# Optimization experiments

Hardware: AMD Instinct MI355X
Metric: run time of the kernel (lower is better)

The kernel has to match this reference:

```python
import jax, jax.numpy as jnp
import numpy as np

HEADS = 4
DIM_HEAD = 32
DIM = HEADS * DIM_HEAD  # 128
B, H, W, C = 32, 64, 64, 128
LN_EPS = 1e-5


def setup_inputs() -> dict:
    key = jax.random.key(0)
    k0, k1, k2, k3, k4 = jax.random.split(key, 5)
    x = jax.random.normal(k0, (B, H, W, C), dtype=jnp.float32)
    # 1x1 convs are pointwise dense layers over channels
    w_qkv = jax.random.normal(k1, (C, DIM * 3), dtype=jnp.float32) * (1.0 / np.sqrt(C))
    w_out = jax.random.normal(k2, (DIM, C), dtype=jnp.float32) * (1.0 / np.sqrt(DIM))
    b_out = jax.random.normal(k3, (C,), dtype=jnp.float32) * 0.01
    ln_scale = jnp.ones((C,), dtype=jnp.float32)
    return {"x": x, "w_qkv": w_qkv, "w_out": w_out, "b_out": b_out, "ln_scale": ln_scale}


def reference(x, w_qkv, w_out, b_out, ln_scale):
    b, h, w, c = x.shape
    n = h * w
    # qkv projection (1x1 conv, no bias)
    qkv = jnp.einsum('bhwc,cf->bhwf', x, w_qkv)  # [B,H,W,3*DIM]
    q, k, v = jnp.split(qkv, 3, axis=-1)
    # rearrange 'b x y (h d) -> b (x y) h d'
    q = q.reshape(b, n, HEADS, DIM_HEAD)
    k = k.reshape(b, n, HEADS, DIM_HEAD)
    v = v.reshape(b, n, HEADS, DIM_HEAD)
    q = jax.nn.softmax(q, axis=-1) * (1.0 / np.sqrt(DIM_HEAD))
    k = jax.nn.softmax(k, axis=1)  # softmax over spatial positions
    v = v * (1.0 / n)
    # per-head context: [B, heads, d, e]
    context = jnp.einsum('bnhd,bnhe->bhde', k, v)
    # out: 'b h d e, b n h d -> b h e n', then rearrange 'b h e (x y) -> b x y (h e)'
    out = jnp.einsum('bhde,bnhd->bnhe', context, q)  # [B, n, heads, e]
    out = out.reshape(b, h, w, DIM)  # channel order = (h e), matching rearrange
    # output 1x1 conv (with bias)
    out = jnp.einsum('bhwd,dc->bhwc', out, w_out) + b_out
    # LayerNorm over channels, eps=1e-5, no bias
    mu = jnp.mean(out, axis=-1, keepdims=True)
    var = jnp.mean(jnp.square(out - mu), axis=-1, keepdims=True)
    out = (out - mu) * jax.lax.rsqrt(var + LN_EPS) * ln_scale
    return out
```

## Files before the change

kernel.cpp:

```cpp
#include <hip/hip_runtime.h>
#include <hip/hip_bf16.h>

typedef __attribute__((ext_vector_type(4))) float f32x4;
typedef __attribute__((ext_vector_type(8))) short bf16x8;

#define OFF_QS    0ull
#define OFF_EK    33554432ull
#define OFF_VV    67108864ull
#define OFF_PCTX  100663296ull
#define OFF_PSE   109051904ull
#define OFF_CTXG  109314048ull
#define OFF_WQT   109576192ull
#define OFF_WOT   109674496ull

static __device__ __forceinline__ unsigned short f2bf(float f) {
  unsigned int u = __builtin_bit_cast(unsigned int, f);
  return (unsigned short)((u + 0x7fffu + ((u >> 16) & 1u)) >> 16);
}

static __device__ __forceinline__ void unpack8(uint4 u, float* p) {
  p[0] = __builtin_bit_cast(float, u.x << 16);
  p[1] = __builtin_bit_cast(float, u.x & 0xffff0000u);
  p[2] = __builtin_bit_cast(float, u.y << 16);
  p[3] = __builtin_bit_cast(float, u.y & 0xffff0000u);
  p[4] = __builtin_bit_cast(float, u.z << 16);
  p[5] = __builtin_bit_cast(float, u.z & 0xffff0000u);
  p[6] = __builtin_bit_cast(float, u.w << 16);
  p[7] = __builtin_bit_cast(float, u.w & 0xffff0000u);
}

__global__ __launch_bounds__(256) void k_prep(const float* __restrict__ wqkv,
                                              const float* __restrict__ wout,
                                              unsigned short* __restrict__ wqT,
                                              unsigned short* __restrict__ woT) {
  int idx = blockIdx.x * 256 + threadIdx.x;
  if (idx < 49152) {
    int f = idx >> 7, k = idx & 127;
    wqT[idx] = f2bf(wqkv[k * 384 + f]);
  } else {
    int j = idx - 49152;
    int c = j >> 7, k = j & 127;
    woT[j] = f2bf(wout[k * 128 + c]);
  }
}

__global__ __launch_bounds__(512, 2) void k_qkv(const float* __restrict__ x,
                                                const unsigned short* __restrict__ wqT,
                                                unsigned short* __restrict__ qs,
                                                unsigned short* __restrict__ ek,
                                                unsigned short* __restrict__ vv) {
  extern __shared__ char lds[];
  char* lds_w = lds;
  char* lds_a = lds + 98304;

  const int tid = threadIdx.x;
  const long rowbase = (long)blockIdx.x * 128;

  {
    const int4* src = (const int4*)wqT;
    int4* dst = (int4*)lds_w;
#pragma unroll
    for (int i = 0; i < 12; i++) {
      int u = tid + i * 512;
      dst[u ^ ((u >> 4) & 7)] = src[u];
    }
  }
  {
    const f32x4* src = (const f32x4*)(x + rowbase * 128);
#pragma unroll
    for (int i = 0; i < 8; i++) {
      int u = tid + i * 512;
      f32x4 val = src[u];
      ushort4 bq;
      bq.x = f2bf(val.x); bq.y = f2bf(val.y); bq.z = f2bf(val.z); bq.w = f2bf(val.w);
      int ba = (u * 8) ^ (((u >> 5) & 7) << 4);
      *(ushort4*)(lds_a + ba) = bq;
    }
  }
  __syncthreads();

  const int lane = tid & 63;
  const int g = lane >> 4, c = lane & 15;
  const int wave = tid >> 6;
  const int wm = wave >> 2, wf = wave & 3;

  f32x4 acc[4][6];
#pragma unroll
  for (int mt = 0; mt < 4; mt++)
#pragma unroll
    for (int ft = 0; ft < 6; ft++)
      acc[mt][ft] = (f32x4){0.f, 0.f, 0.f, 0.f};

#pragma unroll
  for (int kk = 0; kk < 4; kk++) {
    const int koff = (kk * 32 + g * 8) * 2;
    bf16x8 af[4], bfrag[6];
#pragma unroll
    for (int mt = 0; mt < 4; mt++) {
      int row = wm * 64 + mt * 16 + c;
      af[mt] = *(const bf16x8*)(lds_a + ((row * 256 + koff) ^ ((row & 7) << 4)));
    }
#pragma unroll
    for (int ft = 0; ft < 6; ft++) {
      int frow = wf * 96 + ft * 16 + c;
      bfrag[ft] = *(const bf16x8*)(lds_w + ((frow * 256 + koff) ^ ((frow & 7) << 4)));
    }
#pragma unroll
    for (int mt = 0; mt < 4; mt++)
#pragma unroll
      for (int ft = 0; ft < 6; ft++)
        acc[mt][ft] = __builtin_amdgcn_mfma_f32_16x16x32_bf16(af[mt], bfrag[ft], acc[mt][ft], 0, 0, 0);
  }

  const float RS32 = 0.17677669529663687f;
#pragma unroll
  for (int ch = 0; ch < 3; ch++) {
    int gc = wf * 96 + ch * 32;
    int sec = gc >> 7;
    int sc = gc & 127;
    unsigned short* dstp = (sec == 0) ? qs : (sec == 1 ? ek : vv);
#pragma unroll
    for (int mt = 0; mt < 4; mt++) {
      f32x4 a0 = acc[mt][2 * ch];
      f32x4 a1 = acc[mt][2 * ch + 1];
      long row0 = rowbase + wm * 64 + mt * 16 + g * 4;
      if (sec == 0) {
#pragma unroll
        for (int r = 0; r < 4; r++) {
          float e0 = __expf(a0[r]), e1 = __expf(a1[r]);
          float s = e0 + e1;
          s += __shfl_xor(s, 1); s += __shfl_xor(s, 2);
          s += __shfl_xor(s, 4); s += __shfl_xor(s, 8);
          float inv = RS32 / s;
          long base = (row0 + r) * 128 + sc + c;
          dstp[base]      = f2bf(e0 * inv);
          dstp[base + 16] = f2bf(e1 * inv);
        }
      } else if (sec == 1) {
#pragma unroll
        for (int r = 0; r < 4; r++) {
          long base = (row0 + r) * 128 + sc + c;
          dstp[base]      = f2bf(__expf(a0[r]));
          dstp[base + 16] = f2bf(__expf(a1[r]));
        }
      } else {
#pragma unroll
        for (int r = 0; r < 4; r++) {
          long base = (row0 + r) * 128 + sc + c;
          dstp[base]      = f2bf(a0[r]);
          dstp[base + 16] = f2bf(a1[r]);
        }
      }
    }
  }
}

__global__ __launch_bounds__(256) void k_ctx(const unsigned short* __restrict__ ek,
                                             const unsigned short* __restrict__ vv,
                                             float* __restrict__ pctx,
                                             float* __restrict__ pse) {
  extern __shared__ char lds[];
  float* ekc = (float*)lds;
  float* vcc = (float*)(lds + 32768);

  const int tid = threadIdx.x;
  const int chunk = blockIdx.x, b = blockIdx.y;
  const long row0 = (long)b * 4096 + chunk * 256;
  const int wave = tid >> 6, lane = tid & 63;
  const int d0 = (lane >> 3) * 4, e0 = (lane & 7) * 4;
  const int nn = tid >> 2, part = tid & 3;

  f32x4 acc0 = {0.f,0.f,0.f,0.f}, acc1 = {0.f,0.f,0.f,0.f};
  f32x4 acc2 = {0.f,0.f,0.f,0.f}, acc3 = {0.f,0.f,0.f,0.f};
  f32x4 se   = {0.f,0.f,0.f,0.f};

  for (int s = 0; s < 4; s++) {
    long r = row0 + s * 64 + nn;
#pragma unroll
    for (int h = 0; h < 4; h++) {
      uint4 ue = *(const uint4*)(ek + r * 128 + h * 32 + part * 8);
      uint4 uv = *(const uint4*)(vv + r * 128 + h * 32 + part * 8);
      unpack8(ue, &ekc[(h * 64 + nn) * 32 + part * 8]);
      unpack8(uv, &vcc[(h * 64 + nn) * 32 + part * 8]);
    }
    __syncthreads();
    const float* eb = &ekc[(wave * 64) * 32];
    const float* vb = &vcc[(wave * 64) * 32];
#pragma unroll 4
    for (int n = 0; n < 64; n++) {
      f32x4 ev  = *(const f32x4*)(eb + n * 32 + d0);
      f32x4 v4  = *(const f32x4*)(vb + n * 32 + e0);
      acc0 += ev.x * v4;
      acc1 += ev.y * v4;
      acc2 += ev.z * v4;
      acc3 += ev.w * v4;
      se += ev;
    }
    __syncthreads();
  }
  const long pb = ((long)chunk * 128 + b * 4 + wave) * 1024;
  *(f32x4*)&pctx[pb + (d0 + 0) * 32 + e0] = acc0;
  *(f32x4*)&pctx[pb + (d0 + 1) * 32 + e0] = acc1;
  *(f32x4*)&pctx[pb + (d0 + 2) * 32 + e0] = acc2;
  *(f32x4*)&pctx[pb + (d0 + 3) * 32 + e0] = acc3;
  if ((lane & 7) == 0)
    *(f32x4*)&pse[((long)chunk * 128 + b * 4 + wave) * 32 + d0] = se;
}

__global__ __launch_bounds__(256) void k_ctxred(const float* __restrict__ pctx,
                                                const float* __restrict__ pse,
                                                unsigned short* __restrict__ ctxg) {
  int idx = blockIdx.x * 256 + threadIdx.x;
  int de = idx & 1023, d = de >> 5, bh = idx >> 10;
  float s = 0.f, sume = 0.f;
#pragma unroll
  for (int ch = 0; ch < 16; ch++) {
    s    += pctx[(ch * 128 + bh) * 1024 + de];
    sume += pse[(ch * 128 + bh) * 32 + d];
  }
  ctxg[idx] = f2bf(s / (sume * 4096.0f));
}

__global__ __launch_bounds__(512, 2) void k_out(const unsigned short* __restrict__ qs,
                                                const unsigned short* __restrict__ ctxg,
                                                const unsigned short* __restrict__ woT,
                                                const float* __restrict__ bout,
                                                const float* __restrict__ lnsc,
                                                float* __restrict__ out) {
  extern __shared__ char lds[];
  char* lds_wo = lds;
  char* lds_at = lds + 32768;
  unsigned short* lds_cx = (unsigned short*)(lds + 65536);
  float* lds_bias  = (float*)(lds + 73728);
  float* lds_scale = (float*)(lds + 74240);

  const int tid = threadIdx.x;
  const long rowbase = (long)blockIdx.x * 128;
  const int b = blockIdx.x >> 5;

  {
    const int4* src = (const int4*)woT;
    int4* dst = (int4*)lds_wo;
#pragma unroll
    for (int i = 0; i < 4; i++) {
      int u = tid + i * 512;
      dst[u ^ ((u >> 4) & 7)] = src[u];
    }
  }
  {
    const unsigned int* src = (const unsigned int*)(ctxg + (long)b * 4096);
#pragma unroll
    for (int i = 0; i < 4; i++) {
      int u = tid + i * 512;
      unsigned int w = src[u];
      int j = u * 2;
      int e = j & 31, d = (j >> 5) & 31, h = j >> 10;
      lds_cx[(h * 32 + e) * 32 + d]     = (unsigned short)(w & 0xffffu);
      lds_cx[(h * 32 + e + 1) * 32 + d] = (unsigned short)(w >> 16);
    }
  }
  if (tid < 128) { lds_bias[tid] = bout[tid]; lds_scale[tid] = lnsc[tid]; }
  __syncthreads();

  const int lane = tid & 63, g = lane >> 4, c = lane & 15;
  const int wave = tid >> 6;

  f32x4 acc1[4][2];
#pragma unroll
  for (int h = 0; h < 4; h++) { acc1[h][0] = (f32x4){0.f,0.f,0.f,0.f}; acc1[h][1] = (f32x4){0.f,0.f,0.f,0.f}; }
  const unsigned short* qrow = qs + (rowbase + wave * 16 + c) * 128;
#pragma unroll
  for (int h = 0; h < 4; h++) {
    bf16x8 a = *(const bf16x8*)(qrow + h * 32 + g * 8);
#pragma unroll
    for (int et = 0; et < 2; et++) {
      bf16x8 bq = *(const bf16x8*)(lds_cx + (h * 32 + et * 16 + c) * 32 + g * 8);
      acc1[h][et] = __builtin_amdgcn_mfma_f32_16x16x32_bf16(a, bq, acc1[h][et], 0, 0, 0);
    }
  }
  {
    int rowl = wave * 16 + g * 4;
#pragma unroll
    for (int h = 0; h < 4; h++)
#pragma unroll
      for (int et = 0; et < 2; et++) {
        int col = (2 * h + et) * 16 + c;
#pragma unroll
        for (int r = 0; r < 4; r++) {
          int row = rowl + r;
          int ba = (row * 256 + col * 2) ^ ((row & 7) << 4);
          *(unsigned short*)(lds_at + ba) = f2bf(acc1[h][et][r]);
        }
      }
  }
  __syncthreads();

  f32x4 acc2[8];
#pragma unroll
  for (int ct = 0; ct < 8; ct++) acc2[ct] = (f32x4){0.f,0.f,0.f,0.f};
#pragma unroll
  for (int kk = 0; kk < 4; kk++) {
    int koff = (kk * 32 + g * 8) * 2;
    int arow = wave * 16 + c;
    bf16x8 a = *(const bf16x8*)(lds_at + ((arow * 256 + koff) ^ ((arow & 7) << 4)));
#pragma unroll
    for (int ct = 0; ct < 8; ct++) {
      int wrow = ct * 16 + c;
      bf16x8 bw = *(const bf16x8*)(lds_wo + ((wrow * 256 + koff) ^ ((wrow & 7) << 4)));
      acc2[ct] = __builtin_amdgcn_mfma_f32_16x16x32_bf16(a, bw, acc2[ct], 0, 0, 0);
    }
  }

  float biasv[8], scalev[8];
#pragma unroll
  for (int ct = 0; ct < 8; ct++) { biasv[ct] = lds_bias[ct * 16 + c]; scalev[ct] = lds_scale[ct * 16 + c]; }
#pragma unroll
  for (int ct = 0; ct < 8; ct++)
#pragma unroll
    for (int r = 0; r < 4; r++)
      acc2[ct][r] += biasv[ct];

#pragma unroll
  for (int r = 0; r < 4; r++) {
    float s = 0.f, ss = 0.f;
#pragma unroll
    for (int ct = 0; ct < 8; ct++) { float v = acc2[ct][r]; s += v; ss += v * v; }
    s  += __shfl_xor(s, 1);  s  += __shfl_xor(s, 2);  s  += __shfl_xor(s, 4);  s  += __shfl_xor(s, 8);
    ss += __shfl_xor(ss, 1); ss += __shfl_xor(ss, 2); ss += __shfl_xor(ss, 4); ss += __shfl_xor(ss, 8);
    float mu = s * 0.0078125f;
    float var = ss * 0.0078125f - mu * mu;
    float rstd = rsqrtf(var + 1e-5f);
    long row = rowbase + wave * 16 + g * 4 + r;
#pragma unroll
    for (int ct = 0; ct < 8; ct++)
      out[row * 128 + ct * 16 + c] = (acc2[ct][r] - mu) * rstd * scalev[ct];
  }
}

extern "C" void kernel_launch(void* const* d_in, const int* in_sizes, int n_in,
                              void* d_out, int out_size, void* d_ws, size_t ws_size,
                              hipStream_t stream) {
  (void)in_sizes; (void)n_in; (void)out_size; (void)ws_size;
  const float* x     = (const float*)d_in[0];
  const float* wqkv  = (const float*)d_in[1];
  const float* wout  = (const float*)d_in[2];
  const float* bo    = (const float*)d_in[3];
  const float* lnsc  = (const float*)d_in[4];
  float* out = (float*)d_out;

  char* ws = (char*)d_ws;
  unsigned short* qs   = (unsigned short*)(ws + OFF_QS);
  unsigned short* ek   = (unsigned short*)(ws + OFF_EK);
  unsigned short* vv   = (unsigned short*)(ws + OFF_VV);
  float*          pctx = (float*)(ws + OFF_PCTX);
  float*          pse  = (float*)(ws + OFF_PSE);
  unsigned short* ctxg = (unsigned short*)(ws + OFF_CTXG);
  unsigned short* wqT  = (unsigned short*)(ws + OFF_WQT);
  unsigned short* woT  = (unsigned short*)(ws + OFF_WOT);

  k_prep<<<dim3(256), dim3(256), 0, stream>>>(wqkv, wout, wqT, woT);
  k_qkv<<<dim3(1024), dim3(512), 131072, stream>>>(x, wqT, qs, ek, vv);
  k_ctx<<<dim3(16, 32), dim3(256), 65536, stream>>>(ek, vv, pctx, pse);
  k_ctxred<<<dim3(512), dim3(256), 0, stream>>>(pctx, pse, ctxg);
  k_out<<<dim3(1024), dim3(512), 74752, stream>>>(qs, ctxg, woT, bo, lnsc, out);
}
```

Measured before the change: 226.1 us.

## Fuse K/V context accumulation into QKV projection kernel via LDS and MFMA

The QKV projection kernel now also computes per-head exp(K)^T V partial context with MFMA, reading from an LDS transpose, plus the exp(K) column sums. This removes the global writes and re-reads of the ek and vv intermediates (64 MB of bf16) and drops the separate k_ctx kernel. Each block now handles 512 rows over four 128-row tiles and prefetches the next x tile into registers. The grid shrinks from 1024 to 256 blocks and each tile gains extra barriers, which may reduce occupancy and latency hiding.

```diff
diff --git a/kernel.cpp b/kernel.cpp
--- a/kernel.cpp
+++ b/kernel.cpp
@@ -5,28 +5,15 @@
 typedef __attribute__((ext_vector_type(8))) short bf16x8;
 
 #define OFF_QS    0ull
-#define OFF_EK    33554432ull
-#define OFF_VV    67108864ull
-#define OFF_PCTX  100663296ull
-#define OFF_PSE   109051904ull
-#define OFF_CTXG  109314048ull
-#define OFF_WQT   109576192ull
-#define OFF_WOT   109674496ull
+#define OFF_PCTX  33554432ull
+#define OFF_PSE   41943040ull
+#define OFF_CTXG  42205184ull
+#define OFF_WQT   42467328ull
+#define OFF_WOT   42565632ull
 
 static __device__ __forceinline__ unsigned short f2bf(float f) {
   unsigned int u = __builtin_bit_cast(unsigned int, f);
   return (unsigned short)((u + 0x7fffu + ((u >> 16) & 1u)) >> 16);
-}
-
-static __device__ __forceinline__ void unpack8(uint4 u, float* p) {
-  p[0] = __builtin_bit_cast(float, u.x << 16);
-  p[1] = __builtin_bit_cast(float, u.x & 0xffff0000u);
-  p[2] = __builtin_bit_cast(float, u.y << 16);
-  p[3] = __builtin_bit_cast(float, u.y & 0xffff0000u);
-  p[4] = __builtin_bit_cast(float, u.z << 16);
-  p[5] = __builtin_bit_cast(float, u.z & 0xffff0000u);
-  p[6] = __builtin_bit_cast(float, u.w << 16);
-  p[7] = __builtin_bit_cast(float, u.w & 0xffff0000u);
 }
 
 __global__ __launch_bounds__(256) void k_prep(const float* __restrict__ wqkv,
@@ -44,17 +31,20 @@
   }
 }
 
-__global__ __launch_bounds__(512, 2) void k_qkv(const float* __restrict__ x,
-                                                const unsigned short* __restrict__ wqT,
-                                                unsigned short* __restrict__ qs,
-                                                unsigned short* __restrict__ ek,
-                                                unsigned short* __restrict__ vv) {
+__global__ __launch_bounds__(512, 2) void k_qkv_fused(const float* __restrict__ x,
+                                                      const unsigned short* __restrict__ wqT,
+                                                      unsigned short* __restrict__ qs,
+                                                      float* __restrict__ pctx,
+                                                      float* __restrict__ pse) {
   extern __shared__ char lds[];
   char* lds_w = lds;
   char* lds_a = lds + 98304;
 
   const int tid = threadIdx.x;
-  const long rowbase = (long)blockIdx.x * 128;
+  const int beta = blockIdx.x;
+  const int lane = tid & 63, g = lane >> 4, c = lane & 15;
+  const int wave = tid >> 6, wm = wave >> 2, wf = wave & 3;
+  const int h_task = wave & 3, ns_task = wave >> 2;
 
   {
     const int4* src = (const int4*)wqT;
@@ -65,158 +55,184 @@
       dst[u ^ ((u >> 4) & 7)] = src[u];
     }
   }
-  {
-    const f32x4* src = (const f32x4*)(x + rowbase * 128);
-#pragma unroll
-    for (int i = 0; i < 8; i++) {
-      int u = tid + i * 512;
-      f32x4 val = src[u];
-      ushort4 bq;
-      bq.x = f2bf(val.x); bq.y = f2bf(val.y); bq.z = f2bf(val.z); bq.w = f2bf(val.w);
-      int ba = (u * 8) ^ (((u >> 5) & 7) << 4);
-      *(ushort4*)(lds_a + ba) = bq;
-    }
-  }
-  __syncthreads();
-
-  const int lane = tid & 63;
-  const int g = lane >> 4, c = lane & 15;
-  const int wave = tid >> 6;
-  const int wm = wave >> 2, wf = wave & 3;
-
-  f32x4 acc[4][6];
-#pragma unroll
-  for (int mt = 0; mt < 4; mt++)
-#pragma unroll
-    for (int ft = 0; ft < 6; ft++)
-      acc[mt][ft] = (f32x4){0.f, 0.f, 0.f, 0.f};
-
-#pragma unroll
-  for (int kk = 0; kk < 4; kk++) {
-    const int koff = (kk * 32 + g * 8) * 2;
-    bf16x8 af[4], bfrag[6];
-#pragma unroll
-    for (int mt = 0; mt < 4; mt++) {
-      int row = wm * 64 + mt * 16 + c;
-      af[mt] = *(const bf16x8*)(lds_a + ((row * 256 + koff) ^ ((row & 7) << 4)));
-    }
-#pragma unroll
-    for (int ft = 0; ft < 6; ft++) {
-      int frow = wf * 96 + ft * 16 + c;
-      bfrag[ft] = *(const bf16x8*)(lds_w + ((frow * 256 + koff) ^ ((frow & 7) << 4)));
-    }
+
+  f32x4 pre[8];
+  {
+    const f32x4* src = (const f32x4*)(x + (long)beta * 512 * 128);
+#pragma unroll
+    for (int i = 0; i < 8; i++) pre[i] = src[i * 512 + tid];
+  }
+
+  f32x4 cacc[2][2];
+#pragma unroll
+  for (int dt = 0; dt < 2; dt++)
+#pragma unroll
+    for (int et = 0; et < 2; et++) cacc[dt][et] = (f32x4){0.f, 0.f, 0.f, 0.f};
+  float seacc[3][2];
+#pragma unroll
+  for (int i = 0; i < 3; i++) { seacc[i][0] = 0.f; seacc[i][1] = 0.f; }
+
+  for (int t = 0; t < 4; t++) {
+    const long rowbase = ((long)beta * 4 + t) * 128;
+    __syncthreads();
+
+    {
+#pragma unroll
+      for (int i = 0; i < 8; i++) {
+        int u = i * 512 + tid;
+        f32x4 val = pre[i];
+        ushort4 bq;
+        bq.x = f2bf(val.x); bq.y = f2bf(val.y); bq.z = f2bf(val.z); bq.w = f2bf(val.w);
+        int ba = (u * 8) ^ (((u >> 5) & 7) << 4);
+        *(ushort4*)(lds_a + ba) = bq;
+      }
+    }
+    if (t < 3) {
+      const f32x4* src = (const f32x4*)(x + (rowbase + 128) * 128);
+#pragma unroll
+      for (int i = 0; i < 8; i++) pre[i] = src[i * 512 + tid];
+    }
+    __syncthreads();
+
+    f32x4 acc[4][6];
 #pragma unroll
     for (int mt = 0; mt < 4; mt++)
 #pragma unroll
-      for (int ft = 0; ft < 6; ft++)
-        acc[mt][ft] = __builtin_amdgcn_mfma_f32_16x16x32_bf16(af[mt], bfrag[ft], acc[mt][ft], 0, 0, 0);
-  }
-
-  const float RS32 = 0.17677669529663687f;
+      for (int ft = 0; ft < 6; ft++) acc[mt][ft] = (f32x4){0.f, 0.f, 0.f, 0.f};
+
+#pragma unroll
+    for (int kk = 0; kk < 4; kk++) {
+      const int koff = (kk * 32 + g * 8) * 2;
+      bf16x8 af[4], bfrag[6];
+#pragma unroll
+      for (int mt = 0; mt < 4; mt++) {
+        int row = wm * 64 + mt * 16 + c;
+        af[mt] = *(const bf16x8*)(lds_a + ((row * 256 + koff) ^ ((row & 7) << 4)));
+      }
+#pragma unroll
+      for (int ft = 0; ft < 6; ft++) {
+        int frow = wf * 96 + ft * 16 + c;
+        bfrag[ft] = *(const bf16x8*)(lds_w + ((frow * 256 + koff) ^ ((frow & 7) << 4)));
+      }
+#pragma unroll
+      for (int mt = 0; mt < 4; mt++)
+#pragma unroll
+        for (int ft = 0; ft < 6; ft++)
+          acc[mt][ft] = __builtin_amdgcn_mfma_f32_16x16x32_bf16(af[mt], bfrag[ft], acc[mt][ft], 0, 0, 0);
+    }
+    __syncthreads();
+
+    const float RS32 = 0.17677669529663687f;
+#pragma unroll
+    for (int half = 0; half < 2; half++) {
+#pragma unroll
+      for (int ch = 0; ch < 3; ch++) {
+        int gc = wf * 96 + ch * 32;
+        int sec = gc >> 7;
+        int sc = gc & 127;
+        int h = (gc & 127) >> 5;
+        if (sec == 0) {
+          if (half == 0) {
+#pragma unroll
+            for (int mt = 0; mt < 4; mt++) {
+              f32x4 a0 = acc[mt][2 * ch], a1 = acc[mt][2 * ch + 1];
+              long row0 = rowbase + wm * 64 + mt * 16 + g * 4;
+#pragma unroll
+              for (int r = 0; r < 4; r++) {
+                float e0 = __expf(a0[r]), e1 = __expf(a1[r]);
+                float s = e0 + e1;
+                s += __shfl_xor(s, 1); s += __shfl_xor(s, 2);
+                s += __shfl_xor(s, 4); s += __shfl_xor(s, 8);
+                float inv = RS32 / s;
+                long base = (row0 + r) * 128 + sc + c;
+                qs[base]      = f2bf(e0 * inv);
+                qs[base + 16] = f2bf(e1 * inv);
+              }
+            }
+          }
+        } else if (wm == half) {
+          char* tbase = lds_a + (sec == 1 ? 0 : 16384) + h * 4096;
+#pragma unroll
+          for (int mt = 0; mt < 4; mt++) {
+            f32x4 a0 = acc[mt][2 * ch], a1 = acc[mt][2 * ch + 1];
+#pragma unroll
+            for (int r = 0; r < 4; r++) {
+              int nl = mt * 16 + g * 4 + r;
+              float v0 = a0[r], v1 = a1[r];
+              if (sec == 1) {
+                v0 = __expf(v0); v1 = __expf(v1);
+                seacc[ch][0] += v0; seacc[ch][1] += v1;
+              }
+              *(unsigned short*)(tbase + ((c * 128 + nl * 2) ^ ((c & 7) << 4))) = f2bf(v0);
+              *(unsigned short*)(tbase + (((c + 16) * 128 + nl * 2) ^ ((c & 7) << 4))) = f2bf(v1);
+            }
+          }
+        }
+      }
+      __syncthreads();
+
+      {
+        const int noff = (ns_task * 32 + g * 8) * 2;
+        bf16x8 afr[2], bfr[2];
+#pragma unroll
+        for (int dt = 0; dt < 2; dt++) {
+          int row = dt * 16 + c;
+          afr[dt] = *(const bf16x8*)(lds_a + h_task * 4096 + ((row * 128 + noff) ^ ((c & 7) << 4)));
+        }
+#pragma unroll
+        for (int et = 0; et < 2; et++) {
+          int row = et * 16 + c;
+          bfr[et] = *(const bf16x8*)(lds_a + 16384 + h_task * 4096 + ((row * 128 + noff) ^ ((c & 7) << 4)));
+        }
+#pragma unroll
+        for (int dt = 0; dt < 2; dt++)
+#pragma unroll
+          for (int et = 0; et < 2; et++)
+            cacc[dt][et] = __builtin_amdgcn_mfma_f32_16x16x32_bf16(afr[dt], bfr[et], cacc[dt][et], 0, 0, 0);
+      }
+      __syncthreads();
+    }
+  }
+
+  {
+    const long pcbase = ((long)beta * 8 + h_task * 2 + ns_task) * 1024;
+#pragma unroll
+    for (int dt = 0; dt < 2; dt++)
+#pragma unroll
+      for (int et = 0; et < 2; et++)
+#pragma unroll
+        for (int r = 0; r < 4; r++)
+          pctx[pcbase + (dt * 16 + g * 4 + r) * 32 + et * 16 + c] = cacc[dt][et][r];
+  }
 #pragma unroll
   for (int ch = 0; ch < 3; ch++) {
     int gc = wf * 96 + ch * 32;
-    int sec = gc >> 7;
-    int sc = gc & 127;
-    unsigned short* dstp = (sec == 0) ? qs : (sec == 1 ? ek : vv);
-#pragma unroll
-    for (int mt = 0; mt < 4; mt++) {
-      f32x4 a0 = acc[mt][2 * ch];
-      f32x4 a1 = acc[mt][2 * ch + 1];
-      long row0 = rowbase + wm * 64 + mt * 16 + g * 4;
-      if (sec == 0) {
-#pragma unroll
-        for (int r = 0; r < 4; r++) {
-          float e0 = __expf(a0[r]), e1 = __expf(a1[r]);
-          float s = e0 + e1;
-          s += __shfl_xor(s, 1); s += __shfl_xor(s, 2);
-          s += __shfl_xor(s, 4); s += __shfl_xor(s, 8);
-          float inv = RS32 / s;
-          long base = (row0 + r) * 128 + sc + c;
-          dstp[base]      = f2bf(e0 * inv);
-          dstp[base + 16] = f2bf(e1 * inv);
-        }
-      } else if (sec == 1) {
-#pragma unroll
-        for (int r = 0; r < 4; r++) {
-          long base = (row0 + r) * 128 + sc + c;
-          dstp[base]      = f2bf(__expf(a0[r]));
-          dstp[base + 16] = f2bf(__expf(a1[r]));
-        }
-      } else {
-#pragma unroll
-        for (int r = 0; r < 4; r++) {
-          long base = (row0 + r) * 128 + sc + c;
-          dstp[base]      = f2bf(a0[r]);
-          dstp[base + 16] = f2bf(a1[r]);
-        }
-      }
-    }
-  }
-}
-
-__global__ __launch_bounds__(256) void k_ctx(const unsigned short* __restrict__ ek,
-                                             const unsigned short* __restrict__ vv,
-                                             float* __restrict__ pctx,
-                                             float* __restrict__ pse) {
-  extern __shared__ char lds[];
-  float* ekc = (float*)lds;
-  float* vcc = (float*)(lds + 32768);
-
-  const int tid = threadIdx.x;
-  const int chunk = blockIdx.x, b = blockIdx.y;
-  const long row0 = (long)b * 4096 + chunk * 256;
-  const int wave = tid >> 6, lane = tid & 63;
-  const int d0 = (lane >> 3) * 4, e0 = (lane & 7) * 4;
-  const int nn = tid >> 2, part = tid & 3;
-
-  f32x4 acc0 = {0.f,0.f,0.f,0.f}, acc1 = {0.f,0.f,0.f,0.f};
-  f32x4 acc2 = {0.f,0.f,0.f,0.f}, acc3 = {0.f,0.f,0.f,0.f};
-  f32x4 se   = {0.f,0.f,0.f,0.f};
-
-  for (int s = 0; s < 4; s++) {
-    long r = row0 + s * 64 + nn;
-#pragma unroll
-    for (int h = 0; h < 4; h++) {
-      uint4 ue = *(const uint4*)(ek + r * 128 + h * 32 + part * 8);
-      uint4 uv = *(const uint4*)(vv + r * 128 + h * 32 + part * 8);
-      unpack8(ue, &ekc[(h * 64 + nn) * 32 + part * 8]);
-      unpack8(uv, &vcc[(h * 64 + nn) * 32 + part * 8]);
-    }
-    __syncthreads();
-    const float* eb = &ekc[(wave * 64) * 32];
-    const float* vb = &vcc[(wave * 64) * 32];
-#pragma unroll 4
-    for (int n = 0; n < 64; n++) {
-      f32x4 ev  = *(const f32x4*)(eb + n * 32 + d0);
-      f32x4 v4  = *(const f32x4*)(vb + n * 32 + e0);
-      acc0 += ev.x * v4;
-      acc1 += ev.y * v4;
-      acc2 += ev.z * v4;
-      acc3 += ev.w * v4;
-      se += ev;
-    }
-    __syncthreads();
-  }
-  const long pb = ((long)chunk * 128 + b * 4 + wave) * 1024;
-  *(f32x4*)&pctx[pb + (d0 + 0) * 32 + e0] = acc0;
-  *(f32x4*)&pctx[pb + (d0 + 1) * 32 + e0] = acc1;
-  *(f32x4*)&pctx[pb + (d0 + 2) * 32 + e0] = acc2;
-  *(f32x4*)&pctx[pb + (d0 + 3) * 32 + e0] = acc3;
-  if ((lane & 7) == 0)
-    *(f32x4*)&pse[((long)chunk * 128 + b * 4 + wave) * 32 + d0] = se;
+    if ((gc >> 7) == 1) {
+      int h = (gc & 127) >> 5;
+      float s0 = seacc[ch][0], s1 = seacc[ch][1];
+      s0 += __shfl_xor(s0, 16); s0 += __shfl_xor(s0, 32);
+      s1 += __shfl_xor(s1, 16); s1 += __shfl_xor(s1, 32);
+      if (lane < 16) {
+        pse[(beta * 8 + h * 2 + wm) * 32 + c]      = s0;
+        pse[(beta * 8 + h * 2 + wm) * 32 + c + 16] = s1;
+      }
+    }
+  }
 }
 
 __global__ __launch_bounds__(256) void k_ctxred(const float* __restrict__ pctx,
                                                 const float* __restrict__ pse,
                                                 unsigned short* __restrict__ ctxg) {
   int idx = blockIdx.x * 256 + threadIdx.x;
-  int de = idx & 1023, d = de >> 5, bh = idx >> 10;
+  int de = idx & 1023, d = de >> 5;
+  int bh = idx >> 10;
+  int b = bh >> 2, h = bh & 3;
   float s = 0.f, sume = 0.f;
 #pragma unroll
-  for (int ch = 0; ch < 16; ch++) {
-    s    += pctx[(ch * 128 + bh) * 1024 + de];
-    sume += pse[(ch * 128 + bh) * 32 + d];
+  for (int i = 0; i < 8; i++) {
+    int base = (b * 8 + i) * 8 + h * 2;
+    s    += pctx[(long)(base + 0) * 1024 + de] + pctx[(long)(base + 1) * 1024 + de];
+    sume += pse[(base + 0) * 32 + d] + pse[(base + 1) * 32 + d];
   }
   ctxg[idx] = f2bf(s / (sume * 4096.0f));
 }
@@ -350,8 +366,6 @@
 
   char* ws = (char*)d_ws;
   unsigned short* qs   = (unsigned short*)(ws + OFF_QS);
-  unsigned short* ek   = (unsigned short*)(ws + OFF_EK);
-  unsigned short* vv   = (unsigned short*)(ws + OFF_VV);
   float*          pctx = (float*)(ws + OFF_PCTX);
   float*          pse  = (float*)(ws + OFF_PSE);
   unsigned short* ctxg = (unsigned short*)(ws + OFF_CTXG);
@@ -359,8 +373,7 @@
   unsigned short* woT  = (unsigned short*)(ws + OFF_WOT);
 
   k_prep<<<dim3(256), dim3(256), 0, stream>>>(wqkv, wout, wqT, woT);
-  k_qkv<<<dim3(1024), dim3(512), 131072, stream>>>(x, wqT, qs, ek, vv);
-  k_ctx<<<dim3(16, 32), dim3(256), 65536, stream>>>(ek, vv, pctx, pse);
+  k_qkv_fused<<<dim3(256), dim3(512), 131072, stream>>>(x, wqT, qs, pctx, pse);
   k_ctxred<<<dim3(512), dim3(256), 0, stream>>>(pctx, pse, ctxg);
   k_out<<<dim3(1024), dim3(512), 74752, stream>>>(qs, ctxg, woT, bo, lnsc, out);
 }
```

Result: slower. 243.8 us (+7.9%).
